# Optimization experiments

Hardware: AMD Instinct MI355X
Metric: run time of the kernel (lower is better)

## Reference

```python
import jax, jax.numpy as jnp
import numpy as np

B, C, H, W = 4, 256, 48, 48
NUM_HEADS = 8
HEAD_DIM = C // NUM_HEADS
LN_EPS = 1e-5


def setup_inputs() -> dict:
    key = jax.random.key(0)
    ks = jax.random.split(key, 12)
    s = 1.0 / np.sqrt(C)
    return {
        "x": jax.random.normal(ks[0], (B, C, H, W), dtype=jnp.float32),
        "context": jax.random.normal(ks[1], (B, C, H, W), dtype=jnp.float32),
        "Wq": jax.random.uniform(ks[2], (C, C), jnp.float32, -s, s),
        "bq": jax.random.uniform(ks[3], (C,), jnp.float32, -s, s),
        "Wk": jax.random.uniform(ks[4], (C, C), jnp.float32, -s, s),
        "bk": jax.random.uniform(ks[5], (C,), jnp.float32, -s, s),
        "Wv": jax.random.uniform(ks[6], (C, C), jnp.float32, -s, s),
        "bv": jax.random.uniform(ks[7], (C,), jnp.float32, -s, s),
        "Wo": jax.random.uniform(ks[8], (C, C), jnp.float32, -s, s),
        "bo": jax.random.uniform(ks[9], (C,), jnp.float32, -s, s),
        "ln_w": jnp.ones((C,), jnp.float32),
        "ln_b": jnp.zeros((C,), jnp.float32),
    }


def reference(x, context, Wq, bq, Wk, bk, Wv, bv, Wo, bo, ln_w, ln_b):
    b, c, h, w = x.shape
    S = h * w
    # [B, S, C] token layout (x.view(B,C,-1).permute(0,2,1))
    x_flat = x.reshape(b, c, S).transpose(0, 2, 1)
    ctx_flat = context.reshape(b, c, S).transpose(0, 2, 1)
    # QKV projections (torch Linear: y = x @ W.T + b)
    q = (x_flat @ Wq.T + bq).reshape(b, S, NUM_HEADS, HEAD_DIM).transpose(0, 2, 1, 3)
    k = (ctx_flat @ Wk.T + bk).reshape(b, S, NUM_HEADS, HEAD_DIM).transpose(0, 2, 1, 3)
    v = (ctx_flat @ Wv.T + bv).reshape(b, S, NUM_HEADS, HEAD_DIM).transpose(0, 2, 1, 3)
    # attention: [B, heads, S, S]
    scores = jnp.einsum("bhqd,bhkd->bhqk", q, k) / np.sqrt(HEAD_DIM)
    attn = jax.nn.softmax(scores, axis=-1)  # dropout is identity in eval mode
    attended = jnp.einsum("bhqk,bhkd->bhqd", attn, v)
    attended = attended.transpose(0, 2, 1, 3).reshape(b, S, c)
    out = attended @ Wo.T + bo
    # residual + layernorm over channel dim
    y = out + x_flat
    mu = jnp.mean(y, axis=-1, keepdims=True)
    var = jnp.var(y, axis=-1, keepdims=True)
    y = (y - mu) * jax.lax.rsqrt(var + LN_EPS) * ln_w + ln_b
    return y.transpose(0, 2, 1).reshape(b, c, h, w)
```

## Files before the change

kernel.cpp:

```cpp
#include <hip/hip_runtime.h>

#define B_ 4
#define C_ 256
#define S_ 2304
#define NH_ 8
#define HD_ 32
#define QS_L2E (0.17677669529663687f * 1.4426950408889634f)

typedef __attribute__((ext_vector_type(8))) __bf16 b16x8;
typedef __attribute__((ext_vector_type(4))) __bf16 b16x4;
typedef __attribute__((ext_vector_type(4))) float f32x4;
typedef __attribute__((ext_vector_type(4))) unsigned u32x4;

static __device__ __forceinline__ f32x4 mfma_bf16(b16x8 a, b16x8 b, f32x4 c) {
  return __builtin_amdgcn_mfma_f32_16x16x32_bf16(a, b, c, 0, 0, 0);
}

__global__ __launch_bounds__(256) void k_cvtw(
    const float* __restrict__ Wq, const float* __restrict__ Wk,
    const float* __restrict__ Wv, const float* __restrict__ Wo,
    __bf16* __restrict__ Wb, __bf16* __restrict__ Wob) {
  const int e = blockIdx.x * 1024 + threadIdx.x * 4;
  const float* s;
  __bf16* d;
  if (e < 196608) {
    const int m = e >> 16;
    s = (m == 0 ? Wq : (m == 1 ? Wk : Wv)) + (e & 65535);
    d = Wb + e;
  } else {
    s = Wo + (e - 196608);
    d = Wob + (e - 196608);
  }
  f32x4 v = *(const f32x4*)s;
  b16x4 o;
#pragma unroll
  for (int j = 0; j < 4; ++j) o[j] = (__bf16)v[j];
  *(b16x4*)d = o;
}

__global__ __launch_bounds__(256) void k_qkv(
    const float* __restrict__ x, const float* __restrict__ ctx,
    const __bf16* __restrict__ Wb,
    const float* __restrict__ bq, const float* __restrict__ bk, const float* __restrict__ bv,
    __bf16* __restrict__ Q, __bf16* __restrict__ Kd, __bf16* __restrict__ Vt) {
  __shared__ __bf16 lx[16][264];
  const int t = threadIdx.x;
  const int wid = t >> 6;
  const int lane = t & 63;
  const int col = lane & 15, g = lane >> 4;
  int r = blockIdx.x;
  const int p = r / 576; r %= 576;
  const int b = r / 144;
  const int s0 = (r % 144) * 16;
  const float* src = (p == 0 ? x : ctx) + (size_t)b * C_ * S_ + s0;
  const __bf16* W = Wb + p * 65536;
  const float* bias = p == 0 ? bq : (p == 1 ? bk : bv);
  const int i0 = wid * 64;
  const __bf16* arow = W + (size_t)(i0 + col) * C_ + g * 8;

  b16x8 af0 = *(const b16x8*)(arow);
  b16x8 af1 = *(const b16x8*)(arow + (size_t)16 * C_);
  b16x8 af2 = *(const b16x8*)(arow + (size_t)32 * C_);
  b16x8 af3 = *(const b16x8*)(arow + (size_t)48 * C_);

  {
    const int cr = t >> 2, sq = (t & 3) * 4;
#pragma unroll
    for (int j = 0; j < 4; ++j) {
      const int c = j * 64 + cr;
      f32x4 v = *(const f32x4*)(src + (size_t)c * S_ + sq);
#pragma unroll
      for (int jj = 0; jj < 4; ++jj) lx[sq + jj][c] = (__bf16)v[jj];
    }
  }
  __syncthreads();

  f32x4 acc[4] = {};
  b16x8 bf = *(const b16x8*)(&lx[col][g * 8]);

  for (int kk = 0; kk < 8; ++kk) {
    const int nk = ((kk + 1) & 7) * 32;
    b16x8 nbf = *(const b16x8*)(&lx[col][nk + g * 8]);
    b16x8 naf0 = *(const b16x8*)(arow + nk);
    b16x8 naf1 = *(const b16x8*)(arow + (size_t)16 * C_ + nk);
    b16x8 naf2 = *(const b16x8*)(arow + (size_t)32 * C_ + nk);
    b16x8 naf3 = *(const b16x8*)(arow + (size_t)48 * C_ + nk);
    __builtin_amdgcn_sched_barrier(0);
    acc[0] = mfma_bf16(af0, bf, acc[0]);
    acc[1] = mfma_bf16(af1, bf, acc[1]);
    acc[2] = mfma_bf16(af2, bf, acc[2]);
    acc[3] = mfma_bf16(af3, bf, acc[3]);
    bf = nbf; af0 = naf0; af1 = naf1; af2 = naf2; af3 = naf3;
  }
  const int tok = s0 + col;
#pragma unroll
  for (int j = 0; j < 4; ++j) {
    const int ib = i0 + j * 16 + g * 4;
    f32x4 bi = *(const f32x4*)(bias + ib);
    const int h = ib >> 5, d0 = ib & 31;
    const size_t bh = (size_t)b * NH_ + h;
    if (p == 2) {
#pragma unroll
      for (int rr = 0; rr < 4; ++rr)
        Vt[(bh * HD_ + d0 + rr) * S_ + tok] = (__bf16)(acc[j][rr] + bi[rr]);
    } else if (p == 1) {
      b16x4 o;
#pragma unroll
      for (int rr = 0; rr < 4; ++rr) o[rr] = (__bf16)(acc[j][rr] + bi[rr]);
      *(b16x4*)(Kd + (bh * S_ + tok) * HD_ + d0) = o;
    } else {
      b16x4 o;
#pragma unroll
      for (int rr = 0; rr < 4; ++rr) o[rr] = (__bf16)((acc[j][rr] + bi[rr]) * QS_L2E);
      *(b16x4*)(Q + (bh * S_ + tok) * HD_ + d0) = o;
    }
  }
}

__global__ __launch_bounds__(256) void k_attn(
    const __bf16* __restrict__ Q, const __bf16* __restrict__ Kd,
    const __bf16* __restrict__ Vt, __bf16* __restrict__ att) {
  __shared__ float mrg[3][2][656];
  int bid = blockIdx.x;
  bid = (bid & 7) * 288 + (bid >> 3);
  const int wid = threadIdx.x >> 6;
  const int lane = threadIdx.x & 63;
  const int col = lane & 15, g = lane >> 4;
  const int bh = bid / 72;
  const int s0 = (bid % 72) * 32;
  const int b = bh >> 3, h = bh & 7;
  const __bf16* Qb = Q + (size_t)bh * S_ * HD_;
  const __bf16* Kb = Kd + (size_t)bh * S_ * HD_;
  const __bf16* Vb = Vt + (size_t)bh * HD_ * S_;

  b16x8 qfr[2];
#pragma unroll
  for (int q = 0; q < 2; ++q)
    qfr[q] = *(const b16x8*)(Qb + (size_t)(s0 + q * 16 + col) * HD_ + g * 8);
  const int kA = ((col >> 2) * 8) + (col & 3);
  const int kbeg = wid * (S_ / 4);

  b16x8 onesf;
#pragma unroll
  for (int j = 0; j < 8; ++j) onesf[j] = (__bf16)1.0f;

  f32x4 acc0[2] = {}, acc1[2] = {}, accl[2] = {};
  const f32x4 zero = {};

  const __bf16* kptr = Kb + (size_t)(kbeg + kA) * HD_ + g * 8;
  const __bf16* vptr = Vb + (size_t)col * S_ + kbeg + g * 8;

  b16x8 ka = *(const b16x8*)(kptr);
  b16x8 kb = *(const b16x8*)(kptr + 4 * HD_);
  b16x8 v0 = *(const b16x8*)(vptr);
  b16x8 v1 = *(const b16x8*)(vptr + 16 * S_);

  for (int it = 0; it < S_ / 4 / 32; ++it) {
    kptr += 32 * HD_; vptr += 32;
    b16x8 ka_n = *(const b16x8*)(kptr);
    b16x8 kb_n = *(const b16x8*)(kptr + 4 * HD_);
    b16x8 v0_n = *(const b16x8*)(vptr);
    b16x8 v1_n = *(const b16x8*)(vptr + 16 * S_);
    __builtin_amdgcn_sched_barrier(0);

#pragma unroll
    for (int q = 0; q < 2; ++q) {
      f32x4 sA = mfma_bf16(ka, qfr[q], zero);
      f32x4 sB = mfma_bf16(kb, qfr[q], zero);
      float eA0 = __builtin_amdgcn_exp2f(sA[0]);
      float eA1 = __builtin_amdgcn_exp2f(sA[1]);
      float eA2 = __builtin_amdgcn_exp2f(sA[2]);
      float eA3 = __builtin_amdgcn_exp2f(sA[3]);
      float eB0 = __builtin_amdgcn_exp2f(sB[0]);
      float eB1 = __builtin_amdgcn_exp2f(sB[1]);
      float eB2 = __builtin_amdgcn_exp2f(sB[2]);
      float eB3 = __builtin_amdgcn_exp2f(sB[3]);
      unsigned w0, w1, w2, w3;
      asm("v_cvt_pk_bf16_f32 %0, %1, %2" : "=v"(w0) : "v"(eA0), "v"(eA1));
      asm("v_cvt_pk_bf16_f32 %0, %1, %2" : "=v"(w1) : "v"(eA2), "v"(eA3));
      asm("v_cvt_pk_bf16_f32 %0, %1, %2" : "=v"(w2) : "v"(eB0), "v"(eB1));
      asm("v_cvt_pk_bf16_f32 %0, %1, %2" : "=v"(w3) : "v"(eB2), "v"(eB3));
      u32x4 pw = {w0, w1, w2, w3};
      b16x8 pf = __builtin_bit_cast(b16x8, pw);
      acc0[q] = mfma_bf16(pf, v0, acc0[q]);
      acc1[q] = mfma_bf16(pf, v1, acc1[q]);
      accl[q] = mfma_bf16(pf, onesf, accl[q]);
    }
    ka = ka_n; kb = kb_n; v0 = v0_n; v1 = v1_n;
  }

  if (wid > 0) {
#pragma unroll
    for (int qt = 0; qt < 2; ++qt) {
      float* m0 = mrg[wid - 1][qt];
      *(f32x4*)(m0 + col * 20 + g * 4) = acc0[qt];
      *(f32x4*)(m0 + 320 + col * 20 + g * 4) = acc1[qt];
      if (col == 0) *(f32x4*)(m0 + 640 + g * 4) = accl[qt];
    }
  }
  __syncthreads();
  if (wid == 0) {
#pragma unroll
    for (int qt = 0; qt < 2; ++qt) {
      f32x4 t0 = acc0[qt], t1 = acc1[qt], tl = accl[qt];
#pragma unroll
      for (int m = 0; m < 3; ++m) {
        const float* pm = mrg[m][qt];
        t0 += *(const f32x4*)(pm + col * 20 + g * 4);
        t1 += *(const f32x4*)(pm + 320 + col * 20 + g * 4);
        tl += *(const f32x4*)(pm + 640 + g * 4);
      }
#pragma unroll
      for (int j = 0; j < 4; ++j) {
        const int q = g * 4 + j;
        const float inv = 1.f / tl[j];
        const size_t obase = ((size_t)b * S_ + s0 + qt * 16 + q) * C_ + h * HD_;
        att[obase + col] = (__bf16)(t0[j] * inv);
        att[obase + 16 + col] = (__bf16)(t1[j] * inv);
      }
    }
  }
}

__global__ __launch_bounds__(256) void k_oln(
    const __bf16* __restrict__ att, const __bf16* __restrict__ Wob,
    const float* __restrict__ bo, const float* __restrict__ x,
    const float* __restrict__ lnw, const float* __restrict__ lnb,
    float* __restrict__ out) {
  __shared__ float part[4][2][16];
  __shared__ float lw[256], lb[256];
  const int wid = threadIdx.x >> 6;
  const int lane = threadIdx.x & 63;
  const int col = lane & 15, g = lane >> 4;
  int r = blockIdx.x;
  const int b = r / 144;
  const int s0 = (r % 144) * 16;
  const int i0 = wid * 64;
  lw[threadIdx.x] = lnw[threadIdx.x];
  lb[threadIdx.x] = lnb[threadIdx.x];

  f32x4 acc[4] = {};
  const __bf16* arow = att + ((size_t)b * S_ + s0 + col) * C_ + g * 8;
  const __bf16* wrow = Wob + (size_t)(i0 + col) * C_ + g * 8;

  b16x8 bfr = *(const b16x8*)(arow);
  b16x8 af0 = *(const b16x8*)(wrow);
  b16x8 af1 = *(const b16x8*)(wrow + (size_t)16 * C_);
  b16x8 af2 = *(const b16x8*)(wrow + (size_t)32 * C_);
  b16x8 af3 = *(const b16x8*)(wrow + (size_t)48 * C_);

  for (int kk = 0; kk < 8; ++kk) {
    const int nk = ((kk + 1) & 7) * 32;
    b16x8 nbfr = *(const b16x8*)(arow + nk);
    b16x8 naf0 = *(const b16x8*)(wrow + nk);
    b16x8 naf1 = *(const b16x8*)(wrow + (size_t)16 * C_ + nk);
    b16x8 naf2 = *(const b16x8*)(wrow + (size_t)32 * C_ + nk);
    b16x8 naf3 = *(const b16x8*)(wrow + (size_t)48 * C_ + nk);
    __builtin_amdgcn_sched_barrier(0);
    acc[0] = mfma_bf16(af0, bfr, acc[0]);
    acc[1] = mfma_bf16(af1, bfr, acc[1]);
    acc[2] = mfma_bf16(af2, bfr, acc[2]);
    acc[3] = mfma_bf16(af3, bfr, acc[3]);
    bfr = nbfr; af0 = naf0; af1 = naf1; af2 = naf2; af3 = naf3;
  }
  float s = 0.f, s2 = 0.f;
#pragma unroll
  for (int j = 0; j < 4; ++j) {
#pragma unroll
    for (int rr = 0; rr < 4; ++rr) {
      const int i = i0 + j * 16 + g * 4 + rr;
      float v = acc[j][rr] + bo[i] + x[((size_t)b * C_ + i) * S_ + s0 + col];
      acc[j][rr] = v;
      s += v; s2 += v * v;
    }
  }
  s += __shfl_xor(s, 16); s2 += __shfl_xor(s2, 16);
  s += __shfl_xor(s, 32); s2 += __shfl_xor(s2, 32);
  if (g == 0) { part[wid][0][col] = s; part[wid][1][col] = s2; }
  __syncthreads();
  float st = part[0][0][col] + part[1][0][col] + part[2][0][col] + part[3][0][col];
  float st2 = part[0][1][col] + part[1][1][col] + part[2][1][col] + part[3][1][col];
  const float mu = st * (1.f / 256.f);
  const float rs = rsqrtf(st2 * (1.f / 256.f) - mu * mu + 1e-5f);
#pragma unroll
  for (int j = 0; j < 4; ++j) {
#pragma unroll
    for (int rr = 0; rr < 4; ++rr) {
      const int i = i0 + j * 16 + g * 4 + rr;
      out[((size_t)b * C_ + i) * S_ + s0 + col] = (acc[j][rr] - mu) * rs * lw[i] + lb[i];
    }
  }
}

extern "C" void kernel_launch(void* const* d_in, const int* in_sizes, int n_in,
                              void* d_out, int out_size, void* d_ws, size_t ws_size,
                              hipStream_t stream) {
  const float* x   = (const float*)d_in[0];
  const float* ctx = (const float*)d_in[1];
  const float* Wq  = (const float*)d_in[2];
  const float* bq  = (const float*)d_in[3];
  const float* Wk  = (const float*)d_in[4];
  const float* bk  = (const float*)d_in[5];
  const float* Wv  = (const float*)d_in[6];
  const float* bv  = (const float*)d_in[7];
  const float* Wo  = (const float*)d_in[8];
  const float* bo  = (const float*)d_in[9];
  const float* lnw = (const float*)d_in[10];
  const float* lnb = (const float*)d_in[11];
  float* out = (float*)d_out;

  char* ws = (char*)d_ws;
  __bf16* Wb  = (__bf16*)(ws + 9437184);
  __bf16* Wob = (__bf16*)(ws + 9830400);
  __bf16* Kd  = (__bf16*)(ws + 9961472);
  __bf16* Vt  = (__bf16*)(ws + 14680064);
  __bf16* att = (__bf16*)(ws + 19398656);
  __bf16* Q   = (__bf16*)(ws + 24117248);

  k_cvtw <<< 256, 256, 0, stream>>>(Wq, Wk, Wv, Wo, Wb, Wob);
  k_qkv  <<<1728, 256, 0, stream>>>(x, ctx, Wb, bq, bk, bv, Q, Kd, Vt);
  k_attn <<<2304, 256, 0, stream>>>(Q, Kd, Vt, att);
  k_oln  <<< 576, 256, 0, stream>>>(att, Wob, bo, x, lnw, lnb, out);
}
```

Baseline: 195.9 us.

## Double attention query tile and use 512-thread blocks for projection GEMMs

The attention kernel now handles 64 queries per block instead of 32. Each K/V fragment load therefore feeds four query tiles, which halves K/V global traffic per query at the cost of more registers and a larger LDS merge buffer. The QKV and output-projection kernels move to 512 threads with 8 waves, each computing 32 output channels. This raises wave-level parallelism and shortens each wave's MFMA chain. Workspace offsets are also compacted to start at zero.

After: 179.3 us. 8.5% less time.

```diff
diff --git a/kernel.cpp b/kernel.cpp
--- a/kernel.cpp
+++ b/kernel.cpp
@@ -38,7 +38,7 @@
   *(b16x4*)d = o;
 }
 
-__global__ __launch_bounds__(256) void k_qkv(
+__global__ __launch_bounds__(512) void k_qkv(
     const float* __restrict__ x, const float* __restrict__ ctx,
     const __bf16* __restrict__ Wb,
     const float* __restrict__ bq, const float* __restrict__ bk, const float* __restrict__ bv,
@@ -55,27 +55,25 @@
   const float* src = (p == 0 ? x : ctx) + (size_t)b * C_ * S_ + s0;
   const __bf16* W = Wb + p * 65536;
   const float* bias = p == 0 ? bq : (p == 1 ? bk : bv);
-  const int i0 = wid * 64;
+  const int i0 = wid * 32;
   const __bf16* arow = W + (size_t)(i0 + col) * C_ + g * 8;
 
   b16x8 af0 = *(const b16x8*)(arow);
   b16x8 af1 = *(const b16x8*)(arow + (size_t)16 * C_);
-  b16x8 af2 = *(const b16x8*)(arow + (size_t)32 * C_);
-  b16x8 af3 = *(const b16x8*)(arow + (size_t)48 * C_);
 
   {
-    const int cr = t >> 2, sq = (t & 3) * 4;
-#pragma unroll
-    for (int j = 0; j < 4; ++j) {
-      const int c = j * 64 + cr;
-      f32x4 v = *(const f32x4*)(src + (size_t)c * S_ + sq);
-#pragma unroll
-      for (int jj = 0; jj < 4; ++jj) lx[sq + jj][c] = (__bf16)v[jj];
+    const int cr = t >> 1, sq = (t & 1) * 8;
+    f32x4 v0 = *(const f32x4*)(src + (size_t)cr * S_ + sq);
+    f32x4 v1 = *(const f32x4*)(src + (size_t)cr * S_ + sq + 4);
+#pragma unroll
+    for (int jj = 0; jj < 4; ++jj) {
+      lx[sq + jj][cr] = (__bf16)v0[jj];
+      lx[sq + 4 + jj][cr] = (__bf16)v1[jj];
     }
   }
   __syncthreads();
 
-  f32x4 acc[4] = {};
+  f32x4 acc[2] = {};
   b16x8 bf = *(const b16x8*)(&lx[col][g * 8]);
 
   for (int kk = 0; kk < 8; ++kk) {
@@ -83,18 +81,14 @@
     b16x8 nbf = *(const b16x8*)(&lx[col][nk + g * 8]);
     b16x8 naf0 = *(const b16x8*)(arow + nk);
     b16x8 naf1 = *(const b16x8*)(arow + (size_t)16 * C_ + nk);
-    b16x8 naf2 = *(const b16x8*)(arow + (size_t)32 * C_ + nk);
-    b16x8 naf3 = *(const b16x8*)(arow + (size_t)48 * C_ + nk);
     __builtin_amdgcn_sched_barrier(0);
     acc[0] = mfma_bf16(af0, bf, acc[0]);
     acc[1] = mfma_bf16(af1, bf, acc[1]);
-    acc[2] = mfma_bf16(af2, bf, acc[2]);
-    acc[3] = mfma_bf16(af3, bf, acc[3]);
-    bf = nbf; af0 = naf0; af1 = naf1; af2 = naf2; af3 = naf3;
+    bf = nbf; af0 = naf0; af1 = naf1;
   }
   const int tok = s0 + col;
 #pragma unroll
-  for (int j = 0; j < 4; ++j) {
+  for (int j = 0; j < 2; ++j) {
     const int ib = i0 + j * 16 + g * 4;
     f32x4 bi = *(const f32x4*)(bias + ib);
     const int h = ib >> 5, d0 = ib & 31;
@@ -120,22 +114,22 @@
 __global__ __launch_bounds__(256) void k_attn(
     const __bf16* __restrict__ Q, const __bf16* __restrict__ Kd,
     const __bf16* __restrict__ Vt, __bf16* __restrict__ att) {
-  __shared__ float mrg[3][2][656];
+  __shared__ float mrg[3][4][656];
   int bid = blockIdx.x;
-  bid = (bid & 7) * 288 + (bid >> 3);
+  bid = (bid & 7) * 144 + (bid >> 3);
   const int wid = threadIdx.x >> 6;
   const int lane = threadIdx.x & 63;
   const int col = lane & 15, g = lane >> 4;
-  const int bh = bid / 72;
-  const int s0 = (bid % 72) * 32;
+  const int bh = bid / 36;
+  const int s0 = (bid % 36) * 64;
   const int b = bh >> 3, h = bh & 7;
   const __bf16* Qb = Q + (size_t)bh * S_ * HD_;
   const __bf16* Kb = Kd + (size_t)bh * S_ * HD_;
   const __bf16* Vb = Vt + (size_t)bh * HD_ * S_;
 
-  b16x8 qfr[2];
-#pragma unroll
-  for (int q = 0; q < 2; ++q)
+  b16x8 qfr[4];
+#pragma unroll
+  for (int q = 0; q < 4; ++q)
     qfr[q] = *(const b16x8*)(Qb + (size_t)(s0 + q * 16 + col) * HD_ + g * 8);
   const int kA = ((col >> 2) * 8) + (col & 3);
   const int kbeg = wid * (S_ / 4);
@@ -144,7 +138,7 @@
 #pragma unroll
   for (int j = 0; j < 8; ++j) onesf[j] = (__bf16)1.0f;
 
-  f32x4 acc0[2] = {}, acc1[2] = {}, accl[2] = {};
+  f32x4 acc0[4] = {}, acc1[4] = {}, accl[4] = {};
   const f32x4 zero = {};
 
   const __bf16* kptr = Kb + (size_t)(kbeg + kA) * HD_ + g * 8;
@@ -164,7 +158,7 @@
     __builtin_amdgcn_sched_barrier(0);
 
 #pragma unroll
-    for (int q = 0; q < 2; ++q) {
+    for (int q = 0; q < 4; ++q) {
       f32x4 sA = mfma_bf16(ka, qfr[q], zero);
       f32x4 sB = mfma_bf16(kb, qfr[q], zero);
       float eA0 = __builtin_amdgcn_exp2f(sA[0]);
@@ -191,7 +185,7 @@
 
   if (wid > 0) {
 #pragma unroll
-    for (int qt = 0; qt < 2; ++qt) {
+    for (int qt = 0; qt < 4; ++qt) {
       float* m0 = mrg[wid - 1][qt];
       *(f32x4*)(m0 + col * 20 + g * 4) = acc0[qt];
       *(f32x4*)(m0 + 320 + col * 20 + g * 4) = acc1[qt];
@@ -201,7 +195,7 @@
   __syncthreads();
   if (wid == 0) {
 #pragma unroll
-    for (int qt = 0; qt < 2; ++qt) {
+    for (int qt = 0; qt < 4; ++qt) {
       f32x4 t0 = acc0[qt], t1 = acc1[qt], tl = accl[qt];
 #pragma unroll
       for (int m = 0; m < 3; ++m) {
@@ -222,50 +216,44 @@
   }
 }
 
-__global__ __launch_bounds__(256) void k_oln(
+__global__ __launch_bounds__(512) void k_oln(
     const __bf16* __restrict__ att, const __bf16* __restrict__ Wob,
     const float* __restrict__ bo, const float* __restrict__ x,
     const float* __restrict__ lnw, const float* __restrict__ lnb,
     float* __restrict__ out) {
-  __shared__ float part[4][2][16];
+  __shared__ float part[8][2][16];
   __shared__ float lw[256], lb[256];
-  const int wid = threadIdx.x >> 6;
-  const int lane = threadIdx.x & 63;
+  const int t = threadIdx.x;
+  const int wid = t >> 6;
+  const int lane = t & 63;
   const int col = lane & 15, g = lane >> 4;
   int r = blockIdx.x;
   const int b = r / 144;
   const int s0 = (r % 144) * 16;
-  const int i0 = wid * 64;
-  lw[threadIdx.x] = lnw[threadIdx.x];
-  lb[threadIdx.x] = lnb[threadIdx.x];
-
-  f32x4 acc[4] = {};
+  const int i0 = wid * 32;
+  if (t < 256) { lw[t] = lnw[t]; lb[t] = lnb[t]; }
+
+  f32x4 acc[2] = {};
   const __bf16* arow = att + ((size_t)b * S_ + s0 + col) * C_ + g * 8;
   const __bf16* wrow = Wob + (size_t)(i0 + col) * C_ + g * 8;
 
   b16x8 bfr = *(const b16x8*)(arow);
   b16x8 af0 = *(const b16x8*)(wrow);
   b16x8 af1 = *(const b16x8*)(wrow + (size_t)16 * C_);
-  b16x8 af2 = *(const b16x8*)(wrow + (size_t)32 * C_);
-  b16x8 af3 = *(const b16x8*)(wrow + (size_t)48 * C_);
 
   for (int kk = 0; kk < 8; ++kk) {
     const int nk = ((kk + 1) & 7) * 32;
     b16x8 nbfr = *(const b16x8*)(arow + nk);
     b16x8 naf0 = *(const b16x8*)(wrow + nk);
     b16x8 naf1 = *(const b16x8*)(wrow + (size_t)16 * C_ + nk);
-    b16x8 naf2 = *(const b16x8*)(wrow + (size_t)32 * C_ + nk);
-    b16x8 naf3 = *(const b16x8*)(wrow + (size_t)48 * C_ + nk);
     __builtin_amdgcn_sched_barrier(0);
     acc[0] = mfma_bf16(af0, bfr, acc[0]);
     acc[1] = mfma_bf16(af1, bfr, acc[1]);
-    acc[2] = mfma_bf16(af2, bfr, acc[2]);
-    acc[3] = mfma_bf16(af3, bfr, acc[3]);
-    bfr = nbfr; af0 = naf0; af1 = naf1; af2 = naf2; af3 = naf3;
+    bfr = nbfr; af0 = naf0; af1 = naf1;
   }
   float s = 0.f, s2 = 0.f;
 #pragma unroll
-  for (int j = 0; j < 4; ++j) {
+  for (int j = 0; j < 2; ++j) {
 #pragma unroll
     for (int rr = 0; rr < 4; ++rr) {
       const int i = i0 + j * 16 + g * 4 + rr;
@@ -278,12 +266,13 @@
   s += __shfl_xor(s, 32); s2 += __shfl_xor(s2, 32);
   if (g == 0) { part[wid][0][col] = s; part[wid][1][col] = s2; }
   __syncthreads();
-  float st = part[0][0][col] + part[1][0][col] + part[2][0][col] + part[3][0][col];
-  float st2 = part[0][1][col] + part[1][1][col] + part[2][1][col] + part[3][1][col];
+  float st = 0.f, st2 = 0.f;
+#pragma unroll
+  for (int m = 0; m < 8; ++m) { st += part[m][0][col]; st2 += part[m][1][col]; }
   const float mu = st * (1.f / 256.f);
   const float rs = rsqrtf(st2 * (1.f / 256.f) - mu * mu + 1e-5f);
 #pragma unroll
-  for (int j = 0; j < 4; ++j) {
+  for (int j = 0; j < 2; ++j) {
 #pragma unroll
     for (int rr = 0; rr < 4; ++rr) {
       const int i = i0 + j * 16 + g * 4 + rr;
@@ -310,15 +299,15 @@
   float* out = (float*)d_out;
 
   char* ws = (char*)d_ws;
-  __bf16* Wb  = (__bf16*)(ws + 9437184);
-  __bf16* Wob = (__bf16*)(ws + 9830400);
-  __bf16* Kd  = (__bf16*)(ws + 9961472);
-  __bf16* Vt  = (__bf16*)(ws + 14680064);
-  __bf16* att = (__bf16*)(ws + 19398656);
-  __bf16* Q   = (__bf16*)(ws + 24117248);
+  __bf16* Wb  = (__bf16*)(ws);
+  __bf16* Wob = (__bf16*)(ws + 393216);
+  __bf16* Kd  = (__bf16*)(ws + 524288);
+  __bf16* Vt  = (__bf16*)(ws + 5242880);
+  __bf16* att = (__bf16*)(ws + 9961472);
+  __bf16* Q   = (__bf16*)(ws + 14680064);
 
   k_cvtw <<< 256, 256, 0, stream>>>(Wq, Wk, Wv, Wo, Wb, Wob);
-  k_qkv  <<<1728, 256, 0, stream>>>(x, ctx, Wb, bq, bk, bv, Q, Kd, Vt);
-  k_attn <<<2304, 256, 0, stream>>>(Q, Kd, Vt, att);
-  k_oln  <<< 576, 256, 0, stream>>>(att, Wob, bo, x, lnw, lnb, out);
-}
+  k_qkv  <<<1728, 512, 0, stream>>>(x, ctx, Wb, bq, bk, bv, Q, Kd, Vt);
+  k_attn <<<1152, 256, 0, stream>>>(Q, Kd, Vt, att);
+  k_oln  <<< 576, 512, 0, stream>>>(att, Wob, bo, x, lnw, lnb, out);
+}
```
